# Optimization experiments

Hardware: AMD Instinct MI355X
Metric: run time of the kernel (lower is better)

## Reference

```python
import jax, jax.numpy as jnp
import numpy as np

B, DIM, EMBDIM = 32, 512, 512
MEMSIZE, MEMSEQ = 32, 64
VOCAB = 50257


def setup_inputs() -> dict:
    key = jax.random.key(0)
    ks = jax.random.split(key, 10)
    inp = {
        'enc': jax.random.normal(ks[0], (B, DIM), jnp.float32),
        'encsumm': jax.random.normal(ks[1], (B, DIM), jnp.float32),
        'embsumm': jax.random.normal(ks[2], (B, EMBDIM), jnp.float32),
        'memencs': jax.random.normal(ks[3], (B, MEMSIZE, MEMSEQ, DIM), jnp.float32),
        'memencsumm': jax.random.normal(ks[4], (B, MEMSIZE, MEMSEQ, DIM), jnp.float32),
        'memembsumm': jax.random.normal(ks[5], (B, MEMSIZE, MEMSEQ, EMBDIM), jnp.float32),
        'memmask': jnp.ones((B, MEMSIZE, MEMSEQ), jnp.float32),
        'memids': jax.random.randint(ks[6], (B, MEMSIZE, MEMSEQ), 0, VOCAB, jnp.int64 if jax.config.jax_enable_x64 else jnp.int32),
        'W_out': jax.random.normal(ks[7], (VOCAB, 2 * DIM), jnp.float32) * 0.02,
        'b_out': jnp.zeros((VOCAB,), jnp.float32),
        'W_mix': jax.random.normal(ks[8], (2, 2 * DIM), jnp.float32) * 0.02,
        'b_mix': jnp.zeros((2,), jnp.float32),
        'unktok_mask': jnp.ones((VOCAB,), jnp.float32),  # no unktoks
    }
    return inp


def reference(enc, encsumm, embsumm, memencs, memencsumm, memembsumm, memmask,
              memids, W_out, b_out, W_mix, b_mix, unktok_mask):
    # copy branch: attention over flattened memory, scatter-add into vocab
    query = jnp.concatenate([embsumm, jnp.zeros_like(encsumm), enc], axis=-1)        # (B, 2*dim+embdim)
    keys = jnp.concatenate([memembsumm, jnp.zeros_like(memencsumm), memencs], axis=-1)  # (B, M, Z, 2*dim+embdim)
    w = jnp.einsum('bd,bmzd->bmz', query, keys) + jnp.log(memmask)
    b = w.shape[0]
    w = w.reshape(b, -1)                                    # (B, M*Z)
    alphas = jax.nn.softmax(w, axis=-1)
    mem_flat = memencs.reshape(b, -1, memencs.shape[-1])    # (B, M*Z, dim)
    mem_enc_summ = jnp.einsum('bm,bmd->bd', alphas, mem_flat)
    toks = memids.reshape(b, -1)                            # (B, M*Z)
    rows = jnp.arange(b)[:, None]
    vocsize = W_out.shape[0]
    probs_mem = jnp.zeros((b, vocsize), alphas.dtype).at[rows, toks].add(alphas)
    # generation branch
    h = jnp.concatenate([encsumm, enc], axis=-1)            # (B, 2*dim)
    logits_gen = h @ W_out.T + b_out + jnp.log(unktok_mask)[None, :]
    probs_gen = jax.nn.softmax(logits_gen, axis=-1)
    # mixer combine
    mix = jax.nn.softmax(h @ W_mix.T + b_mix, axis=-1)      # (B, 2)
    probs = mix[:, 0:1] * probs_gen + mix[:, 1:2] * probs_mem
    # original stack/gather trick: selects probs where nonzero, zeros where zero -> identity
    probs = jnp.where(probs != 0, probs, jnp.zeros_like(probs))
    return probs, mem_enc_summ
```

## Files before the change

kernel.cpp:

```cpp
#include <hip/hip_runtime.h>
#include <hip/hip_bf16.h>

#define NB   32
#define DIMK 512
#define MM   32
#define ZZ   64
#define MZV  2048
#define VOC  50257
#define NK4  1571

typedef __attribute__((ext_vector_type(8))) short  short8;
typedef __attribute__((ext_vector_type(4))) float  f32x4;
typedef __attribute__((ext_vector_type(8))) unsigned short ushort8;

#define WS_W      0
#define WS_PVEC   (WS_W + NB*MZV)
#define WS_LSTAT  (WS_PVEC + NB*MM*DIMK)
#define WS_GSTATW (WS_LSTAT + NB*MM*2)
#define WS_MIX    (WS_GSTATW + NB*2)
#define WS_GPART  (WS_MIX + NB*2)

__device__ __forceinline__ ushort8 cvt8(float4 a, float4 b) {
    union { ushort8 u; __hip_bfloat162 h[4]; } r;
    r.h[0] = __float22bfloat162_rn(make_float2(a.x, a.y));
    r.h[1] = __float22bfloat162_rn(make_float2(a.z, a.w));
    r.h[2] = __float22bfloat162_rn(make_float2(b.x, b.y));
    r.h[3] = __float22bfloat162_rn(make_float2(b.z, b.w));
    return r.u;
}

typedef const __attribute__((address_space(1))) void* gas_t;
typedef __attribute__((address_space(3))) void*       las_t;
__device__ __forceinline__ void gload16(const void* g, void* l) {
    __builtin_amdgcn_global_load_lds((gas_t)g, (las_t)l, 16, 0, 0);
}

__global__ __launch_bounds__(256, 5) void k14_fused(
    const float* __restrict__ enc, const float* __restrict__ embsumm,
    const float* __restrict__ encsumm,
    const float* __restrict__ memencs, const float* __restrict__ memembsumm,
    const float* __restrict__ memmask,
    const float* __restrict__ W_out, const float* __restrict__ b_out,
    const float* __restrict__ unk, float* __restrict__ out,
    float* __restrict__ ws)
{
    __shared__ __align__(16) union {
        struct { float sacc[4][DIMK]; float sst[4][2]; } s1;
        struct { float w[4][1024]; float a[4][1024]; } s4;
    } smem;

    int bid = blockIdx.x;
    int tid = threadIdx.x, wid = tid >> 6, lane = tid & 63;
    bool isK1; int sub;
    if (bid < 2048) { isK1 = ((bid & 1) == 0); sub = bid >> 1; }
    else            { isK1 = false;            sub = bid - 1024; }

    if (isK1) {
        int b = sub >> 5, m = sub & 31;
        int c0 = lane * 4, c1 = c0 + 256;
        const float* encb = enc + b * DIMK;
        const float* embb = embsumm + b * DIMK;
        float4 qe0 = *(const float4*)(encb + c0);
        float4 qe1 = *(const float4*)(encb + c1);
        float4 qm0 = *(const float4*)(embb + c0);
        float4 qm1 = *(const float4*)(embb + c1);
        const float* meb = memencs    + (long)(b*MM + m) * ZZ * DIMK;
        const float* mmb = memembsumm + (long)(b*MM + m) * ZZ * DIMK;
        const float* mkb = memmask    + (long)(b*MM + m) * ZZ;
        float* w_ws = ws + WS_W + b*MZV + m*ZZ;

        float lmax = -3.0e38f, lsum = 0.f;
        float4 a0 = make_float4(0.f,0.f,0.f,0.f), a1 = make_float4(0.f,0.f,0.f,0.f);

        for (int z = wid; z < ZZ; z += 4) {
            const float* mer = meb + z*DIMK;
            const float* mmr = mmb + z*DIMK;
            float4 e0 = *(const float4*)(mer + c0);
            float4 e1 = *(const float4*)(mer + c1);
            float4 s0 = *(const float4*)(mmr + c0);
            float4 s1 = *(const float4*)(mmr + c1);
            float d = e0.x*qe0.x + e0.y*qe0.y + e0.z*qe0.z + e0.w*qe0.w
                    + e1.x*qe1.x + e1.y*qe1.y + e1.z*qe1.z + e1.w*qe1.w
                    + s0.x*qm0.x + s0.y*qm0.y + s0.z*qm0.z + s0.w*qm0.w
                    + s1.x*qm1.x + s1.y*qm1.y + s1.z*qm1.z + s1.w*qm1.w;
            #pragma unroll
            for (int off = 32; off; off >>= 1) d += __shfl_xor(d, off);
            d += logf(mkb[z]);
            if (lane == 0) w_ws[z] = d;
            float nm = fmaxf(lmax, d);
            float sc = __expf(lmax - nm);
            float e  = __expf(d - nm);
            lsum = lsum * sc + e;
            a0.x = a0.x*sc + e*e0.x; a0.y = a0.y*sc + e*e0.y;
            a0.z = a0.z*sc + e*e0.z; a0.w = a0.w*sc + e*e0.w;
            a1.x = a1.x*sc + e*e1.x; a1.y = a1.y*sc + e*e1.y;
            a1.z = a1.z*sc + e*e1.z; a1.w = a1.w*sc + e*e1.w;
            lmax = nm;
        }

        *(float4*)&smem.s1.sacc[wid][c0] = a0;
        *(float4*)&smem.s1.sacc[wid][c1] = a1;
        if (lane == 0) { smem.s1.sst[wid][0] = lmax; smem.s1.sst[wid][1] = lsum; }
        __syncthreads();
        float bm = fmaxf(fmaxf(smem.s1.sst[0][0], smem.s1.sst[1][0]),
                         fmaxf(smem.s1.sst[2][0], smem.s1.sst[3][0]));
        float sc0 = __expf(smem.s1.sst[0][0]-bm), sc1 = __expf(smem.s1.sst[1][0]-bm);
        float sc2 = __expf(smem.s1.sst[2][0]-bm), sc3 = __expf(smem.s1.sst[3][0]-bm);
        float bs = smem.s1.sst[0][1]*sc0 + smem.s1.sst[1][1]*sc1
                 + smem.s1.sst[2][1]*sc2 + smem.s1.sst[3][1]*sc3;
        int d0 = tid * 2;
        float2 v0 = *(float2*)&smem.s1.sacc[0][d0];
        float2 v1 = *(float2*)&smem.s1.sacc[1][d0];
        float2 v2 = *(float2*)&smem.s1.sacc[2][d0];
        float2 v3 = *(float2*)&smem.s1.sacc[3][d0];
        float p0 = v0.x*sc0 + v1.x*sc1 + v2.x*sc2 + v3.x*sc3;
        float p1 = v0.y*sc0 + v1.y*sc1 + v2.y*sc2 + v3.y*sc3;
        float* pv = ws + WS_PVEC + (long)(b*MM+m)*DIMK + d0;
        pv[0] = p0; pv[1] = p1;
        if (tid == 0) { float* ls = ws + WS_LSTAT + (b*MM+m)*2; ls[0] = bm; ls[1] = bs; }
    } else {
        int wv = wid >> 1, wb = wid & 1;
        int vt = sub * 32;

        int srow = tid >> 3, sq = tid & 7;
        int sqs = sq ^ (srow & 7);
        const float* wbase = W_out + (long)min(vt + srow, VOC-1)*1024 + sqs*4;
        int aoff = srow*DIMK + sqs*4;
        int ldst = tid * 4;

#define ISSUE(ch, bf) do {                                                   \
            gload16(wbase + (ch)*32, &smem.s4.w[bf][ldst]);                  \
            const float* asp = (((ch) < 16) ? encsumm : enc) + aoff + ((ch)&15)*32; \
            gload16(asp, &smem.s4.a[bf][ldst]); } while (0)

        int lg = lane >> 4, ln = lane & 15;
        int vrow = wv*16 + ln;
        int ab   = wb*16 + ln;
        int wq0 = (vrow*8 + ((lg*2)     ^ (vrow & 7))) * 4;
        int wq1 = (vrow*8 + ((lg*2 + 1) ^ (vrow & 7))) * 4;
        int aq0 = (ab*8   + ((lg*2)     ^ (ab & 7)))   * 4;
        int aq1 = (ab*8   + ((lg*2 + 1) ^ (ab & 7)))   * 4;
        f32x4 acc = {0.f, 0.f, 0.f, 0.f};

        ISSUE(0, 0); ISSUE(1, 1); ISSUE(2, 2);

        for (int c = 0; c < 32; ++c) {
            if (c <= 29)      asm volatile("s_waitcnt vmcnt(4)" ::: "memory");
            else if (c == 30) asm volatile("s_waitcnt vmcnt(2)" ::: "memory");
            else              asm volatile("s_waitcnt vmcnt(0)" ::: "memory");
            __builtin_amdgcn_s_barrier();
            if (c + 3 < 32) ISSUE(c + 3, (c + 3) & 3);
            int bf = c & 3;
            float4 b0 = *(const float4*)&smem.s4.w[bf][wq0];
            float4 b1 = *(const float4*)&smem.s4.w[bf][wq1];
            float4 a0 = *(const float4*)&smem.s4.a[bf][aq0];
            float4 a1 = *(const float4*)&smem.s4.a[bf][aq1];
            ushort8 bu = cvt8(b0, b1);
            ushort8 au = cvt8(a0, a1);
            acc = __builtin_amdgcn_mfma_f32_16x16x32_bf16(*(short8*)&au, *(short8*)&bu,
                                                          acc, 0, 0, 0);
        }
#undef ISSUE

        int v = vt + vrow;
        if (v < VOC) {
            float bias = b_out[v] + logf(unk[v]);
            #pragma unroll
            for (int rr = 0; rr < 4; ++rr) {
                int m = wb*16 + lg*4 + rr;
                out[(long)m*VOC + v] = acc[rr] + bias;
            }
        }
    }
}

__global__ __launch_bounds__(256) void k2k5(
    const float* __restrict__ encsumm, const float* __restrict__ enc,
    const float* __restrict__ W_mix, const float* __restrict__ b_mix,
    float* __restrict__ out, float* __restrict__ ws)
{
    int bid = blockIdx.x, tid = threadIdx.x;
    if (bid < 32) {
        int b = bid;
        const float* ls = ws + WS_LSTAT + b*MM*2;
        float gm = -3.0e38f;
        #pragma unroll
        for (int m = 0; m < MM; m++) gm = fmaxf(gm, ls[m*2]);
        float gs = 0.f;
        #pragma unroll
        for (int m = 0; m < MM; m++) gs += ls[m*2+1] * __expf(ls[m*2] - gm);
        if (tid == 0) { ws[WS_GSTATW + b*2] = gm; ws[WS_GSTATW + b*2 + 1] = gs; }
        float inv = 1.0f / gs;
        int d0 = tid * 2;
        float p0 = 0.f, p1 = 0.f;
        for (int m = 0; m < MM; m++) {
            float sc = __expf(ls[m*2] - gm);
            const float* pv = ws + WS_PVEC + (long)(b*MM+m)*DIMK + d0;
            p0 += pv[0]*sc; p1 += pv[1]*sc;
        }
        out[(long)NB*VOC + b*DIMK + d0]     = p0 * inv;
        out[(long)NB*VOC + b*DIMK + d0 + 1] = p1 * inv;

        if (tid < 64) {
            int l = tid;
            float m0 = 0.f, m1 = 0.f;
            #pragma unroll
            for (int p = 0; p < 4; p++) {
                int cc = l*4 + p*256;
                float4 h4 = (cc < 512) ? *(const float4*)(encsumm + b*DIMK + cc)
                                       : *(const float4*)(enc + b*DIMK + cc - 512);
                float4 w0 = *(const float4*)(W_mix + cc);
                float4 w1 = *(const float4*)(W_mix + 1024 + cc);
                m0 += h4.x*w0.x + h4.y*w0.y + h4.z*w0.z + h4.w*w0.w;
                m1 += h4.x*w1.x + h4.y*w1.y + h4.z*w1.z + h4.w*w1.w;
            }
            #pragma unroll
            for (int off = 32; off; off >>= 1) { m0 += __shfl_xor(m0, off); m1 += __shfl_xor(m1, off); }
            if (l == 0) {
                m0 += b_mix[0]; m1 += b_mix[1];
                float mx = fmaxf(m0, m1);
                float e0 = __expf(m0-mx), e1 = __expf(m1-mx);
                float s = e0 + e1;
                ws[WS_MIX + b*2] = e0/s; ws[WS_MIX + b*2 + 1] = e1/s;
            }
        }
    } else {
        int sub = bid - 32;
        int chunk = sub & 31, b = sub >> 5;
        const float* logits = out;
        const int CH = (VOC + 31) / 32;
        int v0 = chunk * CH;
        int v1 = min(VOC, v0 + CH);
        float m = -3.0e38f, s = 0.f;
        for (int v = v0 + tid; v < v1; v += 256) {
            float x = logits[(long)b*VOC + v];
            float nm = fmaxf(m, x);
            s = s*__expf(m - nm) + __expf(x - nm);
            m = nm;
        }
        #pragma unroll
        for (int off = 32; off; off >>= 1) {
            float om = __shfl_xor(m, off), os = __shfl_xor(s, off);
            float nm = fmaxf(m, om);
            s = s*__expf(m - nm) + os*__expf(om - nm);
            m = nm;
        }
        __shared__ float sm[4], ssum[4];
        int wid = tid >> 6, lane = tid & 63;
        if (lane == 0) { sm[wid] = m; ssum[wid] = s; }
        __syncthreads();
        if (tid == 0) {
            float gm = fmaxf(fmaxf(sm[0], sm[1]), fmaxf(sm[2], sm[3]));
            float gs = ssum[0]*__expf(sm[0]-gm) + ssum[1]*__expf(sm[1]-gm)
                     + ssum[2]*__expf(sm[2]-gm) + ssum[3]*__expf(sm[3]-gm);
            ws[WS_GPART + (b*32 + chunk)*2]     = gm;
            ws[WS_GPART + (b*32 + chunk)*2 + 1] = gs;
        }
    }
}

__global__ __launch_bounds__(256) void k6_final(float* __restrict__ probs, const float* __restrict__ ws)
{
    int v = blockIdx.x*256 + threadIdx.x;
    int b = blockIdx.y;
    float gm = -3.0e38f;
    #pragma unroll
    for (int i = 0; i < 32; ++i) gm = fmaxf(gm, ws[WS_GPART + (b*32+i)*2]);
    float gs = 0.f;
    #pragma unroll
    for (int i = 0; i < 32; ++i)
        gs += ws[WS_GPART + (b*32+i)*2 + 1] * __expf(ws[WS_GPART + (b*32+i)*2] - gm);
    if (v >= VOC) return;
    float mix0 = ws[WS_MIX + b*2];
    long idx = (long)b*VOC + v;
    probs[idx] = mix0 * __expf(probs[idx] - gm) / gs;
}

__global__ __launch_bounds__(256) void k7_scatter(const int* __restrict__ memids,
                                                  const float* __restrict__ ws,
                                                  float* __restrict__ probs)
{
    int idx = blockIdx.x*256 + threadIdx.x;
    int b = idx >> 11, mz = idx & 2047;
    float gm = ws[WS_GSTATW + b*2], gs = ws[WS_GSTATW + b*2 + 1];
    float mix1 = ws[WS_MIX + b*2 + 1];
    float alpha = __expf(ws[WS_W + b*MZV + mz] - gm) / gs;
    int tok = memids[b*MZV + mz];
    atomicAdd(&probs[(long)b*VOC + tok], mix1 * alpha);
}

extern "C" void kernel_launch(void* const* d_in, const int* in_sizes, int n_in,
                              void* d_out, int out_size, void* d_ws, size_t ws_size,
                              hipStream_t stream)
{
    const float* enc        = (const float*)d_in[0];
    const float* encsumm    = (const float*)d_in[1];
    const float* embsumm    = (const float*)d_in[2];
    const float* memencs    = (const float*)d_in[3];
    const float* memembsumm = (const float*)d_in[5];
    const float* memmask    = (const float*)d_in[6];
    const int*   memids     = (const int*)d_in[7];
    const float* W_out      = (const float*)d_in[8];
    const float* b_out      = (const float*)d_in[9];
    const float* W_mix      = (const float*)d_in[10];
    const float* b_mix      = (const float*)d_in[11];
    const float* unk        = (const float*)d_in[12];
    float* out = (float*)d_out;
    float* ws  = (float*)d_ws;

    hipLaunchKernelGGL(k14_fused, dim3(1024 + NK4), dim3(256), 0, stream,
                       enc, embsumm, encsumm, memencs, memembsumm, memmask,
                       W_out, b_out, unk, out, ws);
    hipLaunchKernelGGL(k2k5, dim3(32 + 1024), dim3(256), 0, stream,
                       encsumm, enc, W_mix, b_mix, out, ws);
    hipLaunchKernelGGL(k6_final, dim3((VOC + 255)/256, NB), dim3(256), 0, stream, out, ws);
    hipLaunchKernelGGL(k7_scatter, dim3(NB*MZV/256), dim3(256), 0, stream, memids, ws, out);
}
```

Measured before the change: 132.2 us.

## Replace LDS-staged 16x16 MFMA GEMV with split-K 32x32 MFMA and atomic reduction

```diff
diff --git a/kernel.cpp b/kernel.cpp
--- a/kernel.cpp
+++ b/kernel.cpp
@@ -9,9 +9,10 @@
 #define VOC  50257
 #define NK4  1571
 
-typedef __attribute__((ext_vector_type(8))) short  short8;
-typedef __attribute__((ext_vector_type(4))) float  f32x4;
-typedef __attribute__((ext_vector_type(8))) unsigned short ushort8;
+typedef __attribute__((ext_vector_type(8)))  short  short8;
+typedef __attribute__((ext_vector_type(4)))  float  f32x4;
+typedef __attribute__((ext_vector_type(16))) float  f32x16;
+typedef __attribute__((ext_vector_type(8)))  unsigned short ushort8;
 
 #define WS_W      0
 #define WS_PVEC   (WS_W + NB*MZV)
@@ -29,25 +30,15 @@
     return r.u;
 }
 
-typedef const __attribute__((address_space(1))) void* gas_t;
-typedef __attribute__((address_space(3))) void*       las_t;
-__device__ __forceinline__ void gload16(const void* g, void* l) {
-    __builtin_amdgcn_global_load_lds((gas_t)g, (las_t)l, 16, 0, 0);
-}
-
-__global__ __launch_bounds__(256, 5) void k14_fused(
+__global__ __launch_bounds__(256, 6) void k14_fused(
     const float* __restrict__ enc, const float* __restrict__ embsumm,
     const float* __restrict__ encsumm,
     const float* __restrict__ memencs, const float* __restrict__ memembsumm,
     const float* __restrict__ memmask,
-    const float* __restrict__ W_out, const float* __restrict__ b_out,
-    const float* __restrict__ unk, float* __restrict__ out,
+    const float* __restrict__ W_out, float* __restrict__ out,
     float* __restrict__ ws)
 {
-    __shared__ __align__(16) union {
-        struct { float sacc[4][DIMK]; float sst[4][2]; } s1;
-        struct { float w[4][1024]; float a[4][1024]; } s4;
-    } smem;
+    __shared__ __align__(16) struct { float sacc[4][DIMK]; float sst[4][2]; } s1;
 
     int bid = blockIdx.x;
     int tid = threadIdx.x, wid = tid >> 6, lane = tid & 63;
@@ -78,11 +69,11 @@
             float4 e0 = *(const float4*)(mer + c0);
             float4 e1 = *(const float4*)(mer + c1);
             float4 s0 = *(const float4*)(mmr + c0);
-            float4 s1 = *(const float4*)(mmr + c1);
+            float4 s1v = *(const float4*)(mmr + c1);
             float d = e0.x*qe0.x + e0.y*qe0.y + e0.z*qe0.z + e0.w*qe0.w
                     + e1.x*qe1.x + e1.y*qe1.y + e1.z*qe1.z + e1.w*qe1.w
                     + s0.x*qm0.x + s0.y*qm0.y + s0.z*qm0.z + s0.w*qm0.w
-                    + s1.x*qm1.x + s1.y*qm1.y + s1.z*qm1.z + s1.w*qm1.w;
+                    + s1v.x*qm1.x + s1v.y*qm1.y + s1v.z*qm1.z + s1v.w*qm1.w;
             #pragma unroll
             for (int off = 32; off; off >>= 1) d += __shfl_xor(d, off);
             d += logf(mkb[z]);
@@ -98,77 +89,57 @@
             lmax = nm;
         }
 
-        *(float4*)&smem.s1.sacc[wid][c0] = a0;
-        *(float4*)&smem.s1.sacc[wid][c1] = a1;
-        if (lane == 0) { smem.s1.sst[wid][0] = lmax; smem.s1.sst[wid][1] = lsum; }
+        *(float4*)&s1.sacc[wid][c0] = a0;
+        *(float4*)&s1.sacc[wid][c1] = a1;
+        if (lane == 0) { s1.sst[wid][0] = lmax; s1.sst[wid][1] = lsum; }
         __syncthreads();
-        float bm = fmaxf(fmaxf(smem.s1.sst[0][0], smem.s1.sst[1][0]),
-                         fmaxf(smem.s1.sst[2][0], smem.s1.sst[3][0]));
-        float sc0 = __expf(smem.s1.sst[0][0]-bm), sc1 = __expf(smem.s1.sst[1][0]-bm);
-        float sc2 = __expf(smem.s1.sst[2][0]-bm), sc3 = __expf(smem.s1.sst[3][0]-bm);
-        float bs = smem.s1.sst[0][1]*sc0 + smem.s1.sst[1][1]*sc1
-                 + smem.s1.sst[2][1]*sc2 + smem.s1.sst[3][1]*sc3;
+        float bm = fmaxf(fmaxf(s1.sst[0][0], s1.sst[1][0]),
+                         fmaxf(s1.sst[2][0], s1.sst[3][0]));
+        float sc0 = __expf(s1.sst[0][0]-bm), sc1 = __expf(s1.sst[1][0]-bm);
+        float sc2 = __expf(s1.sst[2][0]-bm), sc3 = __expf(s1.sst[3][0]-bm);
+        float bs = s1.sst[0][1]*sc0 + s1.sst[1][1]*sc1
+                 + s1.sst[2][1]*sc2 + s1.sst[3][1]*sc3;
         int d0 = tid * 2;
-        float2 v0 = *(float2*)&smem.s1.sacc[0][d0];
-        float2 v1 = *(float2*)&smem.s1.sacc[1][d0];
-        float2 v2 = *(float2*)&smem.s1.sacc[2][d0];
-        float2 v3 = *(float2*)&smem.s1.sacc[3][d0];
+        float2 v0 = *(float2*)&s1.sacc[0][d0];
+        float2 v1 = *(float2*)&s1.sacc[1][d0];
+        float2 v2 = *(float2*)&s1.sacc[2][d0];
+        float2 v3 = *(float2*)&s1.sacc[3][d0];
         float p0 = v0.x*sc0 + v1.x*sc1 + v2.x*sc2 + v3.x*sc3;
         float p1 = v0.y*sc0 + v1.y*sc1 + v2.y*sc2 + v3.y*sc3;
         float* pv = ws + WS_PVEC + (long)(b*MM+m)*DIMK + d0;
         pv[0] = p0; pv[1] = p1;
         if (tid == 0) { float* ls = ws + WS_LSTAT + (b*MM+m)*2; ls[0] = bm; ls[1] = bs; }
     } else {
-        int wv = wid >> 1, wb = wid & 1;
         int vt = sub * 32;
-
-        int srow = tid >> 3, sq = tid & 7;
-        int sqs = sq ^ (srow & 7);
-        const float* wbase = W_out + (long)min(vt + srow, VOC-1)*1024 + sqs*4;
-        int aoff = srow*DIMK + sqs*4;
-        int ldst = tid * 4;
-
-#define ISSUE(ch, bf) do {                                                   \
-            gload16(wbase + (ch)*32, &smem.s4.w[bf][ldst]);                  \
-            const float* asp = (((ch) < 16) ? encsumm : enc) + aoff + ((ch)&15)*32; \
-            gload16(asp, &smem.s4.a[bf][ldst]); } while (0)
-
-        int lg = lane >> 4, ln = lane & 15;
-        int vrow = wv*16 + ln;
-        int ab   = wb*16 + ln;
-        int wq0 = (vrow*8 + ((lg*2)     ^ (vrow & 7))) * 4;
-        int wq1 = (vrow*8 + ((lg*2 + 1) ^ (vrow & 7))) * 4;
-        int aq0 = (ab*8   + ((lg*2)     ^ (ab & 7)))   * 4;
-        int aq1 = (ab*8   + ((lg*2 + 1) ^ (ab & 7)))   * 4;
-        f32x4 acc = {0.f, 0.f, 0.f, 0.f};
-
-        ISSUE(0, 0); ISSUE(1, 1); ISSUE(2, 2);
-
-        for (int c = 0; c < 32; ++c) {
-            if (c <= 29)      asm volatile("s_waitcnt vmcnt(4)" ::: "memory");
-            else if (c == 30) asm volatile("s_waitcnt vmcnt(2)" ::: "memory");
-            else              asm volatile("s_waitcnt vmcnt(0)" ::: "memory");
-            __builtin_amdgcn_s_barrier();
-            if (c + 3 < 32) ISSUE(c + 3, (c + 3) & 3);
-            int bf = c & 3;
-            float4 b0 = *(const float4*)&smem.s4.w[bf][wq0];
-            float4 b1 = *(const float4*)&smem.s4.w[bf][wq1];
-            float4 a0 = *(const float4*)&smem.s4.a[bf][aq0];
-            float4 a1 = *(const float4*)&smem.s4.a[bf][aq1];
-            ushort8 bu = cvt8(b0, b1);
-            ushort8 au = cvt8(a0, a1);
-            acc = __builtin_amdgcn_mfma_f32_16x16x32_bf16(*(short8*)&au, *(short8*)&bu,
+        int kq = wid;
+        int rc = lane & 31;
+        int kg = lane >> 5;
+
+        long wrow = min(vt + rc, VOC - 1);
+        const float* wp = W_out + wrow*1024 + kq*256 + kg*8;
+        const float* hp = (kq < 2 ? encsumm : enc) + rc*DIMK + (kq & 1)*256 + kg*8;
+
+        f32x16 acc = {0.f,0.f,0.f,0.f,0.f,0.f,0.f,0.f,
+                      0.f,0.f,0.f,0.f,0.f,0.f,0.f,0.f};
+
+        #pragma unroll 4
+        for (int s = 0; s < 16; ++s) {
+            float4 ha0 = *(const float4*)(hp + s*16);
+            float4 ha1 = *(const float4*)(hp + s*16 + 4);
+            float4 wa0 = *(const float4*)(wp + s*16);
+            float4 wa1 = *(const float4*)(wp + s*16 + 4);
+            ushort8 au = cvt8(ha0, ha1);
+            ushort8 wu = cvt8(wa0, wa1);
+            acc = __builtin_amdgcn_mfma_f32_32x32x16_bf16(*(short8*)&au, *(short8*)&wu,
                                                           acc, 0, 0, 0);
         }
-#undef ISSUE
-
-        int v = vt + vrow;
+
+        int v = vt + rc;
         if (v < VOC) {
-            float bias = b_out[v] + logf(unk[v]);
-            #pragma unroll
-            for (int rr = 0; rr < 4; ++rr) {
-                int m = wb*16 + lg*4 + rr;
-                out[(long)m*VOC + v] = acc[rr] + bias;
+            #pragma unroll
+            for (int r = 0; r < 16; ++r) {
+                int m = (r & 3) + 8*(r >> 2) + 4*kg;
+                atomicAdd(&out[(long)m*VOC + v], acc[r]);
             }
         }
     }
@@ -177,6 +148,7 @@
 __global__ __launch_bounds__(256) void k2k5(
     const float* __restrict__ encsumm, const float* __restrict__ enc,
     const float* __restrict__ W_mix, const float* __restrict__ b_mix,
+    const float* __restrict__ b_out, const float* __restrict__ unk,
     float* __restrict__ out, float* __restrict__ ws)
 {
     int bid = blockIdx.x, tid = threadIdx.x;
@@ -233,7 +205,7 @@
         int v1 = min(VOC, v0 + CH);
         float m = -3.0e38f, s = 0.f;
         for (int v = v0 + tid; v < v1; v += 256) {
-            float x = logits[(long)b*VOC + v];
+            float x = logits[(long)b*VOC + v] + b_out[v] + logf(unk[v]);
             float nm = fmaxf(m, x);
             s = s*__expf(m - nm) + __expf(x - nm);
             m = nm;
@@ -259,7 +231,10 @@
     }
 }
 
-__global__ __launch_bounds__(256) void k6_final(float* __restrict__ probs, const float* __restrict__ ws)
+__global__ __launch_bounds__(256) void k6_final(float* __restrict__ probs,
+                                                const float* __restrict__ b_out,
+                                                const float* __restrict__ unk,
+                                                const float* __restrict__ ws)
 {
     int v = blockIdx.x*256 + threadIdx.x;
     int b = blockIdx.y;
@@ -272,8 +247,9 @@
         gs += ws[WS_GPART + (b*32+i)*2 + 1] * __expf(ws[WS_GPART + (b*32+i)*2] - gm);
     if (v >= VOC) return;
     float mix0 = ws[WS_MIX + b*2];
+    float bias = b_out[v] + logf(unk[v]);
     long idx = (long)b*VOC + v;
-    probs[idx] = mix0 * __expf(probs[idx] - gm) / gs;
+    probs[idx] = mix0 * __expf(probs[idx] + bias - gm) / gs;
 }
 
 __global__ __launch_bounds__(256) void k7_scatter(const int* __restrict__ memids,
@@ -308,11 +284,14 @@
     float* out = (float*)d_out;
     float* ws  = (float*)d_ws;
 
+    hipMemsetAsync(out, 0, (size_t)NB * VOC * sizeof(float), stream);
+
     hipLaunchKernelGGL(k14_fused, dim3(1024 + NK4), dim3(256), 0, stream,
                        enc, embsumm, encsumm, memencs, memembsumm, memmask,
-                       W_out, b_out, unk, out, ws);
+                       W_out, out, ws);
     hipLaunchKernelGGL(k2k5, dim3(32 + 1024), dim3(256), 0, stream,
-                       encsumm, enc, W_mix, b_mix, out, ws);
-    hipLaunchKernelGGL(k6_final, dim3((VOC + 255)/256, NB), dim3(256), 0, stream, out, ws);
+                       encsumm, enc, W_mix, b_mix, b_out, unk, out, ws);
+    hipLaunchKernelGGL(k6_final, dim3((VOC + 255)/256, NB), dim3(256), 0, stream,
+                       out, b_out, unk, ws);
     hipLaunchKernelGGL(k7_scatter, dim3(NB*MZV/256), dim3(256), 0, stream, memids, ws, out);
 }
```

Result: slower. 170.2 us (+28.8%).
